# Performance work log

Hardware: AMD Instinct MI355X
Metric: run time of the kernel (lower is better)

The kernel has to match this reference:

```python
import jax, jax.numpy as jnp
import numpy as np

N, E, F, UNITS, K = 50000, 500000, 128, 256, 3


def setup_inputs() -> dict:
    key = jax.random.key(0)
    k1, k2, k3 = jax.random.split(key, 3)
    x = jax.random.normal(k1, (N, F), dtype=jnp.float32)
    edge_index = jax.random.randint(k2, (2, E), 0, N)
    edge_weight = jnp.ones((E,), dtype=jnp.float32)
    kernel = jax.random.normal(k3, (F * (K + 1), UNITS), dtype=jnp.float32) * 0.02
    bias = jnp.zeros((UNITS,), dtype=jnp.float32)
    return {"x": x, "edge_index": edge_index, "edge_weight": edge_weight,
            "kernel": kernel, "bias": bias}


def _gcn_norm_edge(edge_index, edge_weight, num_nodes):
    # renorm=False, improved=False (tf_geometric gcn_norm_edge):
    # symmetric-normalize original edges, THEN append self-loops with weight 1.0
    row, col = edge_index[0], edge_index[1]
    deg = jax.ops.segment_sum(edge_weight, row, num_segments=num_nodes)
    deg_inv_sqrt = jnp.where(deg > 0, 1.0 / jnp.sqrt(jnp.maximum(deg, 1e-12)), 0.0)
    w = deg_inv_sqrt[row] * edge_weight * deg_inv_sqrt[col]
    loop = jnp.arange(num_nodes)
    row = jnp.concatenate([row, loop])
    col = jnp.concatenate([col, loop])
    w = jnp.concatenate([w, jnp.ones((num_nodes,), dtype=w.dtype)])
    return row, col, w


def reference(x, edge_index, edge_weight, kernel, bias):
    n = x.shape[0]
    row, col, w = _gcn_norm_edge(edge_index, edge_weight, n)
    xs = [x]
    for _ in range(K):
        # out[col] += x[row] * w  (gather -> weight -> scatter-sum)
        h = jax.ops.segment_sum(xs[-1][row] * w[:, None], col, num_segments=n)
        xs.append(h)
    h = jnp.concatenate(xs, axis=-1)  # [N, F*(K+1)]
    out = h @ kernel + bias           # [N, UNITS]
    return out
```

## Files before the change

kernel.cpp:

```cpp
#include <hip/hip_runtime.h>

constexpr int NN = 50000;
constexpr int EE = 500000;
constexpr int FF = 128;
constexpr int UU = 256;
constexpr int KK = 512;
constexpr int NB = (NN + 255) / 256;
constexpr int PS = 32;

using bf16x8 = __attribute__((ext_vector_type(8))) short;
using f32x4  = __attribute__((ext_vector_type(4))) float;

__device__ inline float bf2f(unsigned short b) {
    unsigned u = (unsigned)b << 16; float f; __builtin_memcpy(&f, &u, 4); return f;
}
__device__ inline unsigned short f2bf(float f) {
    unsigned u; __builtin_memcpy(&u, &f, 4);
    u = u + 0x7fffu + ((u >> 16) & 1u);
    return (unsigned short)(u >> 16);
}

typedef __attribute__((address_space(1))) const void GASV;
typedef __attribute__((address_space(3))) void LASV;
__device__ inline void gload_lds16(const void* g, void* l) {
    __builtin_amdgcn_global_load_lds((GASV*)g, (LASV*)l, 16, 0, 0);
}


__global__ __launch_bounds__(256) void k_deg_x(const int* __restrict__ row,
                                               const int* __restrict__ col,
                                               const float* __restrict__ ew,
                                               float* __restrict__ deg_p,
                                               int* __restrict__ cnt_p,
                                               int* __restrict__ slot,
                                               const float4* __restrict__ x4,
                                               unsigned short* __restrict__ H) {
    const int i = blockIdx.x * 256 + threadIdx.x;
    if (i < NN * 32) {
        int n = i >> 5, c4 = i & 31;
        float4 v = x4[i];
        ushort4 o;
        o.x = f2bf(v.x); o.y = f2bf(v.y); o.z = f2bf(v.z); o.w = f2bf(v.w);
        *reinterpret_cast<ushort4*>(H + (size_t)n * KK + c4 * 4) = o;
    }
    if (blockIdx.x % 3 == 0) {
        int e = (blockIdx.x / 3) * 256 + threadIdx.x;
        if (e < EE) {
            atomicAdd(&deg_p[(size_t)row[e] * PS], ew[e]);
            slot[e] = atomicAdd(&cnt_p[(size_t)col[e] * PS], 1);
        }
    }
}


__global__ __launch_bounds__(256) void k_scan1(const int* __restrict__ cnt_p,
                                               const float* __restrict__ deg_p,
                                               float* __restrict__ dis,
                                               int* __restrict__ offs,
                                               int* __restrict__ bsum) {
    const int t = threadIdx.x;
    const int gid = blockIdx.x * 256 + t;
    if (gid < NN) {
        float d = deg_p[(size_t)gid * PS];
        dis[gid] = (d > 0.f) ? (1.0f / sqrtf(fmaxf(d, 1e-12f))) : 0.f;
    }
    int v = (gid < NN) ? cnt_p[(size_t)gid * PS] : 0;
    __shared__ int ts[256];
    ts[t] = v; __syncthreads();
    for (int d = 1; d < 256; d <<= 1) {
        int a = ts[t]; int b = (t >= d) ? ts[t - d] : 0;
        __syncthreads(); ts[t] = a + b; __syncthreads();
    }
    if (gid < NN) offs[gid] = ts[t] - v;
    if (t == 255) bsum[blockIdx.x] = ts[255];
}

__global__ __launch_bounds__(256) void k_scan2(int* __restrict__ bsum) {
    const int t = threadIdx.x;
    int v = (t < NB) ? bsum[t] : 0;
    __shared__ int ts[256];
    ts[t] = v; __syncthreads();
    for (int d = 1; d < 256; d <<= 1) {
        int a = ts[t]; int b = (t >= d) ? ts[t - d] : 0;
        __syncthreads(); ts[t] = a + b; __syncthreads();
    }
    if (t < NB) bsum[t] = ts[t] - v;
}

__global__ __launch_bounds__(256) void k_scan3(int* __restrict__ offs,
                                               const int* __restrict__ bsum) {
    const int gid = blockIdx.x * 256 + threadIdx.x;
    if (gid < NN) offs[gid] += bsum[blockIdx.x];
    if (gid == 0) offs[NN] = EE;
}


__global__ __launch_bounds__(256) void k_scatter(const int* __restrict__ row,
                                                 const int* __restrict__ col,
                                                 const float* __restrict__ ew,
                                                 const float* __restrict__ dis,
                                                 const int* __restrict__ offs,
                                                 const int* __restrict__ slot,
                                                 uint2* __restrict__ edata,
                                                 const float* __restrict__ W,
                                                 unsigned short* __restrict__ Wt) {
    const int e = blockIdx.x * 256 + threadIdx.x;
    if (e < EE) {
        int r = row[e], c = col[e];
        int sl = offs[c] + slot[e];
        float wv = dis[r] * ew[e] * dis[c];
        uint2 d; d.x = (unsigned)r; __builtin_memcpy(&d.y, &wv, 4);
        edata[sl] = d;
    }
    if (e < KK * UU) {
        int k = e >> 8, c = e & 255;
        Wt[(size_t)c * KK + k] = f2bf(W[e]);
    }
}


__global__ __launch_bounds__(256) void k_prop(const int* __restrict__ offs,
                                              const uint2* __restrict__ edata,
                                              unsigned short* __restrict__ H,
                                              int sin, int sout) {
    const int wid = (blockIdx.x * 256 + threadIdx.x) >> 6;
    const int lane = threadIdx.x & 63;
    const int g = lane >> 4;
    const int sl = lane & 15;

    const unsigned short* bin = H + (size_t)sin * FF;
    const unsigned short* rowp = bin + (size_t)wid * KK + sl * 8;

    float a[8];
    {
        uint4 s4 = *reinterpret_cast<const uint4*>(rowp);
        const unsigned sw[4] = {s4.x, s4.y, s4.z, s4.w};
#pragma unroll
        for (int j = 0; j < 8; ++j) {
            float v = bf2f((unsigned short)(sw[j >> 1] >> ((j & 1) * 16)));
            a[j] = (g == 0) ? v : 0.f;
        }
    }

    const int beg = offs[wid], end = offs[wid + 1];
    int e = beg + g;
    for (; e + 4 < end; e += 8) {
        uint2 d0 = edata[e], d1 = edata[e + 4];
        float w0, w1; __builtin_memcpy(&w0, &d0.y, 4); __builtin_memcpy(&w1, &d1.y, 4);
        uint4 v0 = *reinterpret_cast<const uint4*>(bin + (size_t)d0.x * KK + sl * 8);
        uint4 v1 = *reinterpret_cast<const uint4*>(bin + (size_t)d1.x * KK + sl * 8);
        const unsigned u0[4] = {v0.x, v0.y, v0.z, v0.w};
        const unsigned u1[4] = {v1.x, v1.y, v1.z, v1.w};
#pragma unroll
        for (int j = 0; j < 8; ++j)
            a[j] += bf2f((unsigned short)(u0[j >> 1] >> ((j & 1) * 16))) * w0
                  + bf2f((unsigned short)(u1[j >> 1] >> ((j & 1) * 16))) * w1;
    }
    if (e < end) {
        uint2 d0 = edata[e];
        float w0; __builtin_memcpy(&w0, &d0.y, 4);
        uint4 v0 = *reinterpret_cast<const uint4*>(bin + (size_t)d0.x * KK + sl * 8);
        const unsigned u0[4] = {v0.x, v0.y, v0.z, v0.w};
#pragma unroll
        for (int j = 0; j < 8; ++j)
            a[j] += bf2f((unsigned short)(u0[j >> 1] >> ((j & 1) * 16))) * w0;
    }

#pragma unroll
    for (int j = 0; j < 8; ++j) {
        a[j] += __shfl_xor(a[j], 16);
        a[j] += __shfl_xor(a[j], 32);
    }

    if (lane < 16) {
        uint4 o;
        o.x = (unsigned)f2bf(a[0]) | ((unsigned)f2bf(a[1]) << 16);
        o.y = (unsigned)f2bf(a[2]) | ((unsigned)f2bf(a[3]) << 16);
        o.z = (unsigned)f2bf(a[4]) | ((unsigned)f2bf(a[5]) << 16);
        o.w = (unsigned)f2bf(a[6]) | ((unsigned)f2bf(a[7]) << 16);
        *reinterpret_cast<uint4*>(H + (size_t)sout * FF + (size_t)wid * KK + sl * 8) = o;
    }
}


__global__ __launch_bounds__(256, 2) void k_gemm(const unsigned short* __restrict__ H,
                                                 const unsigned short* __restrict__ Wt,
                                                 const float* __restrict__ bias,
                                                 float* __restrict__ out) {
    __shared__ __align__(16) char As[2][128 * 128];
    __shared__ __align__(16) char Bs[2][128 * 128];
    const int t = threadIdx.x;
    const int lane = t & 63;
    const int wv = t >> 6;
    const int wm = wv >> 1;
    const int wn = wv & 1;
    const int brow = (blockIdx.x >> 1) * 128;
    const int bcol = (blockIdx.x & 1) * 128;

    const int r8  = lane >> 3;
    const int b16 = (lane & 7) * 16;

    f32x4 acc[4][4] = {};

    auto stage = [&](int buf, int ks) {
#pragma unroll
        for (int i = 0; i < 8; ++i) {
            int c = wv * 8 + i;
            if (c < 16) {
                int r = c * 8 + r8;
                int gr = brow + r; if (gr >= NN) gr = NN - 1;
                const char* src = (const char*)H + (size_t)gr * (KK * 2) + ks * 128
                                  + (b16 ^ ((r & 7) << 4));
                gload_lds16(src, &As[buf][c * 1024]);
            } else {
                int cc = (c - 16) * 8 + r8;
                int gc = bcol + cc;
                const char* src = (const char*)Wt + (size_t)gc * (KK * 2) + ks * 128
                                  + (b16 ^ ((cc & 7) << 4));
                gload_lds16(src, &Bs[buf][(c - 16) * 1024]);
            }
        }
    };

    auto compute = [&](int buf) {
        bf16x8 af[2][4], bfr[2][4];
#pragma unroll
        for (int kk = 0; kk < 2; ++kk) {
#pragma unroll
            for (int f = 0; f < 4; ++f) {
                int r = wm * 64 + f * 16 + (lane & 15);
                int ba = (kk * 64 + (lane >> 4) * 16) ^ ((r & 7) << 4);
                af[kk][f] = *reinterpret_cast<const bf16x8*>(&As[buf][r * 128 + ba]);
                int cc = wn * 64 + f * 16 + (lane & 15);
                int bb = (kk * 64 + (lane >> 4) * 16) ^ ((cc & 7) << 4);
                bfr[kk][f] = *reinterpret_cast<const bf16x8*>(&Bs[buf][cc * 128 + bb]);
            }
        }
#pragma unroll
        for (int kk = 0; kk < 2; ++kk)
#pragma unroll
            for (int fm = 0; fm < 4; ++fm)
#pragma unroll
                for (int fn = 0; fn < 4; ++fn)
                    acc[fm][fn] = __builtin_amdgcn_mfma_f32_16x16x32_bf16(
                        af[kk][fm], bfr[kk][fn], acc[fm][fn], 0, 0, 0);
    };

    stage(0, 0);
    __syncthreads();
    for (int ks = 0; ks < 8; ++ks) {
        if (ks < 7) stage((ks + 1) & 1, ks + 1);
        compute(ks & 1);
        __syncthreads();
    }

#pragma unroll
    for (int fn = 0; fn < 4; ++fn) {
        int col = bcol + wn * 64 + fn * 16 + (lane & 15);
        float bs = bias[col];
#pragma unroll
        for (int fm = 0; fm < 4; ++fm) {
#pragma unroll
            for (int r4 = 0; r4 < 4; ++r4) {
                int grow = brow + wm * 64 + fm * 16 + (lane >> 4) * 4 + r4;
                if (grow < NN)
                    out[(size_t)grow * UU + col] = acc[fm][fn][r4] + bs;
            }
        }
    }
}


extern "C" void kernel_launch(void* const* d_in, const int* in_sizes, int n_in,
                              void* d_out, int out_size, void* d_ws, size_t ws_size,
                              hipStream_t stream) {
    const float* x    = (const float*)d_in[0];
    const int*   ei   = (const int*)d_in[1];
    const float* ew   = (const float*)d_in[2];
    const float* Wk   = (const float*)d_in[3];
    const float* bias = (const float*)d_in[4];
    float* out = (float*)d_out;

    const int* row = ei;
    const int* col = ei + EE;

    char* ws = (char*)d_ws;
    size_t off = 0;
    auto alloc = [&](size_t bytes) {
        size_t o = off;
        off += (bytes + 255) & ~(size_t)255;
        return o;
    };
    float*          deg_p = (float*)(ws + alloc((size_t)NN * PS * sizeof(float)));
    int*            cnt_p = (int*)  (ws + alloc((size_t)NN * PS * sizeof(int)));
    int*            slot  = (int*)  (ws + alloc((size_t)EE * sizeof(int)));
    float*          dis   = (float*)(ws + alloc((size_t)NN * sizeof(float)));
    int*            offs  = (int*)  (ws + alloc((size_t)(NN + 1) * sizeof(int)));
    int*            bsum  = (int*)  (ws + alloc((size_t)256 * sizeof(int)));
    uint2*          edata = (uint2*)(ws + alloc((size_t)EE * sizeof(uint2)));
    unsigned short* Hcat  = (unsigned short*)(ws + alloc((size_t)NN * KK * sizeof(short)));
    unsigned short* Wt    = (unsigned short*)(ws + alloc((size_t)KK * UU * sizeof(short)));

    hipMemsetAsync(deg_p, 0, (size_t)NN * PS * sizeof(float), stream);
    hipMemsetAsync(cnt_p, 0, (size_t)NN * PS * sizeof(int), stream);

    k_deg_x<<<(NN * 32 + 255) / 256, 256, 0, stream>>>(row, col, ew, deg_p, cnt_p,
                                                       slot, (const float4*)x, Hcat);
    k_scan1<<<NB, 256, 0, stream>>>(cnt_p, deg_p, dis, offs, bsum);
    k_scan2<<<1, 256, 0, stream>>>(bsum);
    k_scan3<<<NB, 256, 0, stream>>>(offs, bsum);
    k_scatter<<<(EE + 255) / 256, 256, 0, stream>>>(row, col, ew, dis, offs, slot,
                                                    edata, Wk, Wt);

    const int gprop = NN / 4;
    k_prop<<<gprop, 256, 0, stream>>>(offs, edata, Hcat, 0, 1);
    k_prop<<<gprop, 256, 0, stream>>>(offs, edata, Hcat, 1, 2);
    k_prop<<<gprop, 256, 0, stream>>>(offs, edata, Hcat, 2, 3);

    k_gemm<<<391 * 2, 256, 0, stream>>>(Hcat, Wt, bias, out);
}
```

Baseline: 262.3 us.

## Replace global-atomic CSR counting with chunked LDS histograms and prefix tables

Edge counting per destination node moves from padded global atomics to per-chunk shared-memory histograms. Each block covers 8192 edges and one half of the node range, using two 16-bit counters packed per word. A column-wise prefix over chunks gives each edge a deterministic slot from a chunk prefix plus a local slot. The x-to-bf16 conversion moves into the scatter kernel, and the GEMM block order is remapped so the two column halves of a row tile run close together for L2 reuse. This trades global atomic contention for extra passes over partial and PRE arrays of about 62x25000 words, and relies on per-chunk counts fitting in 16 bits.

Result: no change. 259.2 us (-1.2%).

```diff
diff --git a/kernel.cpp b/kernel.cpp
--- a/kernel.cpp
+++ b/kernel.cpp
@@ -5,8 +5,15 @@
 constexpr int FF = 128;
 constexpr int UU = 256;
 constexpr int KK = 512;
-constexpr int NB = (NN + 255) / 256;
-constexpr int PS = 32;
+
+constexpr int CHB   = 13;
+constexpr int CHUNK = 1 << CHB;
+constexpr int NCH   = (EE + CHUNK - 1) / CHUNK;
+constexpr int HALF  = 25000;
+constexpr int HW    = HALF / 2;
+constexpr int NW    = NN / 2;
+constexpr int NBW   = (NW + 255) / 256;
+constexpr int NB    = (NN + 255) / 256;
 
 using bf16x8 = __attribute__((ext_vector_type(8))) short;
 using f32x4  = __attribute__((ext_vector_type(4))) float;
@@ -27,14 +34,107 @@
 }
 
 
-__global__ __launch_bounds__(256) void k_deg_x(const int* __restrict__ row,
-                                               const int* __restrict__ col,
-                                               const float* __restrict__ ew,
-                                               float* __restrict__ deg_p,
-                                               int* __restrict__ cnt_p,
-                                               int* __restrict__ slot,
-                                               const float4* __restrict__ x4,
-                                               unsigned short* __restrict__ H) {
+__global__ __launch_bounds__(256) void k_hist(const int* __restrict__ row,
+                                              const int* __restrict__ col,
+                                              const float* __restrict__ ew,
+                                              float* __restrict__ deg,
+                                              unsigned* __restrict__ partial,
+                                              unsigned short* __restrict__ lslot) {
+    __shared__ unsigned hist[HW];
+    const int b = blockIdx.x >> 1;
+    const int r = blockIdx.x & 1;
+    const int t = threadIdx.x;
+    for (int i = t; i < HW; i += 256) hist[i] = 0;
+    __syncthreads();
+    const int beg = b << CHB;
+    const int end = min(beg + CHUNK, EE);
+    const int base = r * HALF;
+    for (int e = beg + t; e < end; e += 256) {
+        int c = col[e];
+        if (r == 0) atomicAdd(&deg[row[e]], ew[e]);
+        if (c >= base && c < base + HALF) {
+            int wl = (c - base) >> 1;
+            int sh = (c & 1) * 16;
+            unsigned old = atomicAdd(&hist[wl], 1u << sh);
+            lslot[e] = (unsigned short)((old >> sh) & 0xffffu);
+        }
+    }
+    __syncthreads();
+    unsigned* dst = partial + ((size_t)b * 2 + r) * HW;
+    for (int i = t; i < HW; i += 256) dst[i] = hist[i];
+}
+
+
+__global__ __launch_bounds__(256) void k_scan1(const unsigned* __restrict__ partial,
+                                               unsigned* __restrict__ PRE,
+                                               const float* __restrict__ deg,
+                                               float* __restrict__ dis,
+                                               int* __restrict__ offs,
+                                               int* __restrict__ bsum) {
+    const int t = threadIdx.x;
+    const int w = blockIdx.x * 256 + t;
+    unsigned run = 0;
+    if (w < NW) {
+        int r = (w >= HW) ? 1 : 0;
+        int wl = w - r * HW;
+        for (int b = 0; b < NCH; ++b) {
+            PRE[(size_t)b * NW + w] = run;
+            run += partial[((size_t)b * 2 + r) * HW + wl];
+        }
+    }
+    const unsigned lo = run & 0xffffu;
+    const int wsum = (w < NW) ? (int)((run & 0xffffu) + (run >> 16)) : 0;
+    __shared__ int ts[256];
+    ts[t] = wsum; __syncthreads();
+    for (int d = 1; d < 256; d <<= 1) {
+        int a = ts[t]; int bb = (t >= d) ? ts[t - d] : 0;
+        __syncthreads(); ts[t] = a + bb; __syncthreads();
+    }
+    int ex = ts[t] - wsum;
+    if (w < NW) {
+        int n0 = 2 * w, n1 = 2 * w + 1;
+        offs[n0] = ex;
+        offs[n1] = ex + (int)lo;
+        float d0 = deg[n0];
+        dis[n0] = (d0 > 0.f) ? (1.0f / sqrtf(fmaxf(d0, 1e-12f))) : 0.f;
+        float d1 = deg[n1];
+        dis[n1] = (d1 > 0.f) ? (1.0f / sqrtf(fmaxf(d1, 1e-12f))) : 0.f;
+    }
+    if (t == 255) bsum[blockIdx.x] = ts[255];
+}
+
+__global__ __launch_bounds__(256) void k_scan2(int* __restrict__ bsum) {
+    const int t = threadIdx.x;
+    int v = (t < NBW) ? bsum[t] : 0;
+    __shared__ int ts[256];
+    ts[t] = v; __syncthreads();
+    for (int d = 1; d < 256; d <<= 1) {
+        int a = ts[t]; int bb = (t >= d) ? ts[t - d] : 0;
+        __syncthreads(); ts[t] = a + bb; __syncthreads();
+    }
+    if (t < NBW) bsum[t] = ts[t] - v;
+}
+
+__global__ __launch_bounds__(256) void k_scan3(int* __restrict__ offs,
+                                               const int* __restrict__ bsum) {
+    const int gid = blockIdx.x * 256 + threadIdx.x;
+    if (gid < NN) offs[gid] += bsum[gid >> 9];
+    if (gid == 0) offs[NN] = EE;
+}
+
+
+__global__ __launch_bounds__(256) void k_scatter(const int* __restrict__ row,
+                                                 const int* __restrict__ col,
+                                                 const float* __restrict__ ew,
+                                                 const float* __restrict__ dis,
+                                                 const int* __restrict__ offs,
+                                                 const unsigned* __restrict__ PRE,
+                                                 const unsigned short* __restrict__ lslot,
+                                                 uint2* __restrict__ edata,
+                                                 const float4* __restrict__ x4,
+                                                 unsigned short* __restrict__ H,
+                                                 const float* __restrict__ W,
+                                                 unsigned short* __restrict__ Wt) {
     const int i = blockIdx.x * 256 + threadIdx.x;
     if (i < NN * 32) {
         int n = i >> 5, c4 = i & 31;
@@ -43,78 +143,18 @@
         o.x = f2bf(v.x); o.y = f2bf(v.y); o.z = f2bf(v.z); o.w = f2bf(v.w);
         *reinterpret_cast<ushort4*>(H + (size_t)n * KK + c4 * 4) = o;
     }
-    if (blockIdx.x % 3 == 0) {
-        int e = (blockIdx.x / 3) * 256 + threadIdx.x;
-        if (e < EE) {
-            atomicAdd(&deg_p[(size_t)row[e] * PS], ew[e]);
-            slot[e] = atomicAdd(&cnt_p[(size_t)col[e] * PS], 1);
-        }
-    }
-}
-
-
-__global__ __launch_bounds__(256) void k_scan1(const int* __restrict__ cnt_p,
-                                               const float* __restrict__ deg_p,
-                                               float* __restrict__ dis,
-                                               int* __restrict__ offs,
-                                               int* __restrict__ bsum) {
-    const int t = threadIdx.x;
-    const int gid = blockIdx.x * 256 + t;
-    if (gid < NN) {
-        float d = deg_p[(size_t)gid * PS];
-        dis[gid] = (d > 0.f) ? (1.0f / sqrtf(fmaxf(d, 1e-12f))) : 0.f;
-    }
-    int v = (gid < NN) ? cnt_p[(size_t)gid * PS] : 0;
-    __shared__ int ts[256];
-    ts[t] = v; __syncthreads();
-    for (int d = 1; d < 256; d <<= 1) {
-        int a = ts[t]; int b = (t >= d) ? ts[t - d] : 0;
-        __syncthreads(); ts[t] = a + b; __syncthreads();
-    }
-    if (gid < NN) offs[gid] = ts[t] - v;
-    if (t == 255) bsum[blockIdx.x] = ts[255];
-}
-
-__global__ __launch_bounds__(256) void k_scan2(int* __restrict__ bsum) {
-    const int t = threadIdx.x;
-    int v = (t < NB) ? bsum[t] : 0;
-    __shared__ int ts[256];
-    ts[t] = v; __syncthreads();
-    for (int d = 1; d < 256; d <<= 1) {
-        int a = ts[t]; int b = (t >= d) ? ts[t - d] : 0;
-        __syncthreads(); ts[t] = a + b; __syncthreads();
-    }
-    if (t < NB) bsum[t] = ts[t] - v;
-}
-
-__global__ __launch_bounds__(256) void k_scan3(int* __restrict__ offs,
-                                               const int* __restrict__ bsum) {
-    const int gid = blockIdx.x * 256 + threadIdx.x;
-    if (gid < NN) offs[gid] += bsum[blockIdx.x];
-    if (gid == 0) offs[NN] = EE;
-}
-
-
-__global__ __launch_bounds__(256) void k_scatter(const int* __restrict__ row,
-                                                 const int* __restrict__ col,
-                                                 const float* __restrict__ ew,
-                                                 const float* __restrict__ dis,
-                                                 const int* __restrict__ offs,
-                                                 const int* __restrict__ slot,
-                                                 uint2* __restrict__ edata,
-                                                 const float* __restrict__ W,
-                                                 unsigned short* __restrict__ Wt) {
-    const int e = blockIdx.x * 256 + threadIdx.x;
-    if (e < EE) {
-        int r = row[e], c = col[e];
-        int sl = offs[c] + slot[e];
-        float wv = dis[r] * ew[e] * dis[c];
-        uint2 d; d.x = (unsigned)r; __builtin_memcpy(&d.y, &wv, 4);
+    if (i < EE) {
+        int rr = row[i], c = col[i];
+        int b = i >> CHB;
+        unsigned pre = PRE[(size_t)b * NW + (c >> 1)];
+        int sl = offs[c] + (int)((pre >> ((c & 1) * 16)) & 0xffffu) + (int)lslot[i];
+        float wv = dis[rr] * ew[i] * dis[c];
+        uint2 d; d.x = (unsigned)rr; __builtin_memcpy(&d.y, &wv, 4);
         edata[sl] = d;
     }
-    if (e < KK * UU) {
-        int k = e >> 8, c = e & 255;
-        Wt[(size_t)c * KK + k] = f2bf(W[e]);
+    if (i < KK * UU) {
+        int k = i >> 8, c = i & 255;
+        Wt[(size_t)c * KK + k] = f2bf(W[i]);
     }
 }
 
@@ -187,6 +227,12 @@
                                                  const unsigned short* __restrict__ Wt,
                                                  const float* __restrict__ bias,
                                                  float* __restrict__ out) {
+    const int q = blockIdx.x >> 4;
+    const int r = blockIdx.x & 7;
+    const int half = (blockIdx.x >> 3) & 1;
+    const int itile = q * 8 + r;
+    if (itile >= 391) return;
+
     __shared__ __align__(16) char As[2][128 * 128];
     __shared__ __align__(16) char Bs[2][128 * 128];
     const int t = threadIdx.x;
@@ -194,8 +240,8 @@
     const int wv = t >> 6;
     const int wm = wv >> 1;
     const int wn = wv & 1;
-    const int brow = (blockIdx.x >> 1) * 128;
-    const int bcol = (blockIdx.x & 1) * 128;
+    const int brow = itile * 128;
+    const int bcol = half * 128;
 
     const int r8  = lane >> 3;
     const int b16 = (lane & 7) * 16;
@@ -207,10 +253,10 @@
         for (int i = 0; i < 8; ++i) {
             int c = wv * 8 + i;
             if (c < 16) {
-                int r = c * 8 + r8;
-                int gr = brow + r; if (gr >= NN) gr = NN - 1;
+                int rr = c * 8 + r8;
+                int gr = brow + rr; if (gr >= NN) gr = NN - 1;
                 const char* src = (const char*)H + (size_t)gr * (KK * 2) + ks * 128
-                                  + (b16 ^ ((r & 7) << 4));
+                                  + (b16 ^ ((rr & 7) << 4));
                 gload_lds16(src, &As[buf][c * 1024]);
             } else {
                 int cc = (c - 16) * 8 + r8;
@@ -228,9 +274,9 @@
         for (int kk = 0; kk < 2; ++kk) {
 #pragma unroll
             for (int f = 0; f < 4; ++f) {
-                int r = wm * 64 + f * 16 + (lane & 15);
-                int ba = (kk * 64 + (lane >> 4) * 16) ^ ((r & 7) << 4);
-                af[kk][f] = *reinterpret_cast<const bf16x8*>(&As[buf][r * 128 + ba]);
+                int rr = wm * 64 + f * 16 + (lane & 15);
+                int ba = (kk * 64 + (lane >> 4) * 16) ^ ((rr & 7) << 4);
+                af[kk][f] = *reinterpret_cast<const bf16x8*>(&As[buf][rr * 128 + ba]);
                 int cc = wn * 64 + f * 16 + (lane & 15);
                 int bb = (kk * 64 + (lane >> 4) * 16) ^ ((cc & 7) << 4);
                 bfr[kk][f] = *reinterpret_cast<const bf16x8*>(&Bs[buf][cc * 128 + bb]);
@@ -256,15 +302,15 @@
 
 #pragma unroll
     for (int fn = 0; fn < 4; ++fn) {
-        int col = bcol + wn * 64 + fn * 16 + (lane & 15);
-        float bs = bias[col];
+        int cg = bcol + wn * 64 + fn * 16 + (lane & 15);
+        float bs = bias[cg];
 #pragma unroll
         for (int fm = 0; fm < 4; ++fm) {
 #pragma unroll
             for (int r4 = 0; r4 < 4; ++r4) {
                 int grow = brow + wm * 64 + fm * 16 + (lane >> 4) * 4 + r4;
                 if (grow < NN)
-                    out[(size_t)grow * UU + col] = acc[fm][fn][r4] + bs;
+                    out[(size_t)grow * UU + cg] = acc[fm][fn][r4] + bs;
             }
         }
     }
@@ -291,31 +337,31 @@
         off += (bytes + 255) & ~(size_t)255;
         return o;
     };
-    float*          deg_p = (float*)(ws + alloc((size_t)NN * PS * sizeof(float)));
-    int*            cnt_p = (int*)  (ws + alloc((size_t)NN * PS * sizeof(int)));
-    int*            slot  = (int*)  (ws + alloc((size_t)EE * sizeof(int)));
-    float*          dis   = (float*)(ws + alloc((size_t)NN * sizeof(float)));
-    int*            offs  = (int*)  (ws + alloc((size_t)(NN + 1) * sizeof(int)));
-    int*            bsum  = (int*)  (ws + alloc((size_t)256 * sizeof(int)));
-    uint2*          edata = (uint2*)(ws + alloc((size_t)EE * sizeof(uint2)));
-    unsigned short* Hcat  = (unsigned short*)(ws + alloc((size_t)NN * KK * sizeof(short)));
-    unsigned short* Wt    = (unsigned short*)(ws + alloc((size_t)KK * UU * sizeof(short)));
-
-    hipMemsetAsync(deg_p, 0, (size_t)NN * PS * sizeof(float), stream);
-    hipMemsetAsync(cnt_p, 0, (size_t)NN * PS * sizeof(int), stream);
-
-    k_deg_x<<<(NN * 32 + 255) / 256, 256, 0, stream>>>(row, col, ew, deg_p, cnt_p,
-                                                       slot, (const float4*)x, Hcat);
-    k_scan1<<<NB, 256, 0, stream>>>(cnt_p, deg_p, dis, offs, bsum);
+    float*          deg     = (float*)(ws + alloc((size_t)NN * sizeof(float)));
+    float*          dis     = (float*)(ws + alloc((size_t)NN * sizeof(float)));
+    int*            offs    = (int*)  (ws + alloc((size_t)(NN + 1) * sizeof(int)));
+    int*            bsum    = (int*)  (ws + alloc((size_t)256 * sizeof(int)));
+    unsigned*       partial = (unsigned*)(ws + alloc((size_t)NCH * 2 * HW * sizeof(unsigned)));
+    unsigned*       PRE     = (unsigned*)(ws + alloc((size_t)NCH * NW * sizeof(unsigned)));
+    unsigned short* lslot   = (unsigned short*)(ws + alloc((size_t)EE * sizeof(short)));
+    uint2*          edata   = (uint2*)(ws + alloc((size_t)EE * sizeof(uint2)));
+    unsigned short* Hcat    = (unsigned short*)(ws + alloc((size_t)NN * KK * sizeof(short)));
+    unsigned short* Wt      = (unsigned short*)(ws + alloc((size_t)KK * UU * sizeof(short)));
+
+    hipMemsetAsync(deg, 0, (size_t)NN * sizeof(float), stream);
+
+    k_hist<<<NCH * 2, 256, 0, stream>>>(row, col, ew, deg, partial, lslot);
+    k_scan1<<<NBW, 256, 0, stream>>>(partial, PRE, deg, dis, offs, bsum);
     k_scan2<<<1, 256, 0, stream>>>(bsum);
     k_scan3<<<NB, 256, 0, stream>>>(offs, bsum);
-    k_scatter<<<(EE + 255) / 256, 256, 0, stream>>>(row, col, ew, dis, offs, slot,
-                                                    edata, Wk, Wt);
+    k_scatter<<<(NN * 32 + 255) / 256, 256, 0, stream>>>(row, col, ew, dis, offs,
+                                                         PRE, lslot, edata,
+                                                         (const float4*)x, Hcat, Wk, Wt);
 
     const int gprop = NN / 4;
     k_prop<<<gprop, 256, 0, stream>>>(offs, edata, Hcat, 0, 1);
     k_prop<<<gprop, 256, 0, stream>>>(offs, edata, Hcat, 1, 2);
     k_prop<<<gprop, 256, 0, stream>>>(offs, edata, Hcat, 2, 3);
 
-    k_gemm<<<391 * 2, 256, 0, stream>>>(Hcat, Wt, bias, out);
-}
+    k_gemm<<<784, 256, 0, stream>>>(Hcat, Wt, bias, out);
+}
```
